# Optimization experiments

Measured on AMD Instinct MI355X. Metric: run time of the kernel, lower is better.

The kernel has to match this reference:

```python
import jax, jax.numpy as jnp
import numpy as np

N_HEADS = 16
D_EMBED = 1024
N_CROSS = 768
D_HEAD = D_EMBED // N_HEADS


def setup_inputs() -> dict:
    key = jax.random.key(0)
    ks = jax.random.split(key, 10)
    B, S = 2, 2048
    x = jax.random.normal(ks[0], (B, S, D_EMBED), dtype=jnp.float32)
    context = jax.random.normal(ks[1], (B, S, N_CROSS), dtype=jnp.float32)
    sq = 1.0 / np.sqrt(D_EMBED)
    sc = 1.0 / np.sqrt(N_CROSS)
    Wq = jax.random.normal(ks[2], (D_EMBED, D_EMBED), dtype=jnp.float32) * sq
    bq = jnp.zeros((D_EMBED,), dtype=jnp.float32)
    Wk = jax.random.normal(ks[3], (N_CROSS, D_EMBED), dtype=jnp.float32) * sc
    bk = jnp.zeros((D_EMBED,), dtype=jnp.float32)
    Wv = jax.random.normal(ks[4], (N_CROSS, D_EMBED), dtype=jnp.float32) * sc
    bv = jnp.zeros((D_EMBED,), dtype=jnp.float32)
    Wo = jax.random.normal(ks[5], (D_EMBED, D_EMBED), dtype=jnp.float32) * sq
    bo = jnp.zeros((D_EMBED,), dtype=jnp.float32)
    return {"x": x, "context": context, "Wq": Wq, "bq": bq, "Wk": Wk, "bk": bk,
            "Wv": Wv, "bv": bv, "Wo": Wo, "bo": bo}


def reference(x, context, Wq, bq, Wk, bk, Wv, bv, Wo, bo):
    B, S, _ = x.shape

    def split_heads(t):  # [B,S,E] -> [B,H,S,Dh]
        return t.reshape(B, S, N_HEADS, D_HEAD).transpose(0, 2, 1, 3)

    q = split_heads(x @ Wq + bq)
    k = split_heads(context @ Wk + bk)
    v = split_heads(context @ Wv + bv)

    scale = 1.0 / np.sqrt(D_HEAD)
    scores = jnp.einsum('bhqd,bhkd->bhqk', q, k) * scale
    attn = jax.nn.softmax(scores, axis=-1)
    out = jnp.einsum('bhqk,bhkd->bhqd', attn, v)
    out = out.transpose(0, 2, 1, 3).reshape(B, S, D_EMBED)
    return out @ Wo + bo
```

## Files before the change

### kernel.cpp

```cpp
#include <hip/hip_runtime.h>
#include <math.h>


namespace {

typedef short bfr __attribute__((ext_vector_type(8)));
typedef short s4v __attribute__((ext_vector_type(4)));
typedef unsigned u4v __attribute__((ext_vector_type(4)));
typedef float accf __attribute__((ext_vector_type(16)));

#define MFMA32(a, b, c) __builtin_amdgcn_mfma_f32_32x32x16_bf16(a, b, c, 0, 0, 0)

__device__ inline short f2bf(float f) {
    unsigned u = __float_as_uint(f);
    u += 0x7fffu + ((u >> 16) & 1u);
    return (short)(u >> 16);
}
__device__ inline float bf2f(short s) {
    return __uint_as_float(((unsigned)(unsigned short)s) << 16);
}
__device__ inline float fexp2(float x) { return __builtin_amdgcn_exp2f(x); }
__device__ inline accf zero16() {
    accf z;
#pragma unroll
    for (int i = 0; i < 16; ++i) z[i] = 0.f;
    return z;
}
__device__ inline void dma16(const void* g, void* l) {
    __builtin_amdgcn_global_load_lds(
        (const __attribute__((address_space(1))) void*)g,
        (__attribute__((address_space(3))) void*)l, 16, 0, 0);
}

__global__ __launch_bounds__(256) void prep(
    const float* __restrict__ x, const float* __restrict__ ctx,
    short* __restrict__ xb, short* __restrict__ cb,
    const float* __restrict__ Wq, const float* __restrict__ Wk,
    const float* __restrict__ Wv, const float* __restrict__ Wo,
    short* __restrict__ Wqt, short* __restrict__ Wkt,
    short* __restrict__ Wvt, short* __restrict__ Wot) {
    __shared__ short t[64][68];
    const int bx = blockIdx.x;
    if (bx < 7168) {
        int i = bx * 256 + threadIdx.x;
        if (i < 1048576) {
            float4 v = ((const float4*)x)[i];
            s4v p = {f2bf(v.x), f2bf(v.y), f2bf(v.z), f2bf(v.w)};
            ((s4v*)xb)[i] = p;
        } else {
            int j = i - 1048576;
            float4 v = ((const float4*)ctx)[j];
            s4v p = {f2bf(v.x), f2bf(v.y), f2bf(v.z), f2bf(v.w)};
            ((s4v*)cb)[j] = p;
        }
        return;
    }
    const int idx = bx - 7168;
    const int z = idx >> 8, gy = (idx >> 4) & 15, gx = idx & 15;
    const float* W;
    short* Wt;
    int K;
    switch (z) {
        case 0: W = Wq; Wt = Wqt; K = 1024; break;
        case 1: W = Wk; Wt = Wkt; K = 768; break;
        case 2: W = Wv; Wt = Wvt; K = 768; break;
        default: W = Wo; Wt = Wot; K = 1024; break;
    }
    const int k0 = gy * 64;
    if (k0 >= K) return;
    const int tid = threadIdx.x;
    const int n0 = gx * 64;
    const int kr = tid >> 4, nc = (tid & 15) * 4;
#pragma unroll
    for (int rep = 0; rep < 4; ++rep) {
        int k = kr + rep * 16;
        float4 v = *(const float4*)&W[(size_t)(k0 + k) * 1024 + n0 + nc];
        t[nc + 0][k] = f2bf(v.x);
        t[nc + 1][k] = f2bf(v.y);
        t[nc + 2][k] = f2bf(v.z);
        t[nc + 3][k] = f2bf(v.w);
    }
    __syncthreads();
    const int nr = tid >> 4, kc = (tid & 15) * 4;
#pragma unroll
    for (int rep = 0; rep < 4; ++rep) {
        int n = nr + rep * 16;
        s4v p = {t[n][kc], t[n][kc + 1], t[n][kc + 2], t[n][kc + 3]};
        *(s4v*)&Wt[(size_t)(n0 + n) * K + k0 + kc] = p;
    }
}

__global__ __launch_bounds__(256) void gemm_qkv(
    const short* __restrict__ xb, const short* __restrict__ cb,
    const short* __restrict__ Wqt, const short* __restrict__ Wkt,
    const short* __restrict__ Wvt, const float* __restrict__ bq,
    const float* __restrict__ bk, const float* __restrict__ bv,
    short* __restrict__ Qf, short* __restrict__ Kf, short* __restrict__ Vt,
    float qscale) {
    const int z = blockIdx.z;
    const short* A  = (z == 0) ? xb : cb;
    const short* Bt = (z == 0) ? Wqt : ((z == 1) ? Wkt : Wvt);
    const float* bias = (z == 0) ? bq : ((z == 1) ? bk : bv);
    const int K = (z == 0) ? 1024 : 768;
    const int NIT = K / 32;
    const float scale = (z == 0) ? qscale : 1.f;
    short* out = (z == 0) ? Qf : ((z == 1) ? Kf : Vt);

    __shared__ short As[8192];
    __shared__ short Bs[8192];
    const int t = threadIdx.x, lane = t & 63, w = t >> 6;
    const int lm = lane & 31, h2 = lane >> 5;
    const int wm = w & 1, wn = w >> 1;
    const int m0 = blockIdx.y * 128, n0 = blockIdx.x * 128;

    const int st = t ^ ((t >> 3) & 7);
    const int srow = st >> 2, scol = (st & 3) * 8;
    const short* ga = A + (size_t)(m0 + srow) * K + scol;
    const short* gb = Bt + (size_t)(n0 + srow) * K + scol;

    const int xorv = (lm >> 1) & 7;
    const int rA0 = wm * 64 + lm, rB0 = wn * 64 + lm;

    accf acc[2][2] = {zero16(), zero16(), zero16(), zero16()};

    dma16(ga, &As[w * 512]);
    dma16(ga + (size_t)64 * K, &As[2048 + w * 512]);
    dma16(gb, &Bs[w * 512]);
    dma16(gb + (size_t)64 * K, &Bs[2048 + w * 512]);

#pragma unroll 1
    for (int it = 0; it < NIT; ++it) {
        const int p = it & 1;
        __syncthreads();
        if (it + 1 < NIT) {
            const int kt = (it + 1) * 32;
            short* lA = &As[(1 - p) * 4096 + w * 512];
            short* lB = &Bs[(1 - p) * 4096 + w * 512];
            dma16(ga + kt, lA);
            dma16(ga + (size_t)64 * K + kt, lA + 2048);
            dma16(gb + kt, lB);
            dma16(gb + (size_t)64 * K + kt, lB + 2048);
        }
        const short* bA = &As[p * 4096];
        const short* bB = &Bs[p * 4096];
#pragma unroll
        for (int kk8 = 0; kk8 < 4; kk8 += 2) {
            bfr a0 = *(const bfr*)&bA[((rA0 * 4 + h2 + kk8) ^ xorv) * 8];
            bfr a1 = *(const bfr*)&bA[(((rA0 + 32) * 4 + h2 + kk8) ^ xorv) * 8];
            bfr b0 = *(const bfr*)&bB[((rB0 * 4 + h2 + kk8) ^ xorv) * 8];
            bfr b1 = *(const bfr*)&bB[(((rB0 + 32) * 4 + h2 + kk8) ^ xorv) * 8];
            acc[0][0] = MFMA32(a0, b0, acc[0][0]);
            acc[0][1] = MFMA32(a0, b1, acc[0][1]);
            acc[1][0] = MFMA32(a1, b0, acc[1][0]);
            acc[1][1] = MFMA32(a1, b1, acc[1][1]);
        }
    }

#pragma unroll
    for (int nt = 0; nt < 2; ++nt) {
        const int n = n0 + wn * 64 + nt * 32 + lm;
        const float bn = bias[n];
        const int hh = n >> 6, dd = n & 63;
#pragma unroll
        for (int mt = 0; mt < 2; ++mt) {
            const int mbase = m0 + wm * 64 + mt * 32 + 4 * h2;
            if (z != 2) {
                const int cb2 = (dd >> 4) * 512 + ((dd >> 3) & 1) * 256 + (dd & 7);
#pragma unroll
                for (int r = 0; r < 16; ++r) {
                    const int m = mbase + (r & 3) + 8 * (r >> 2);
                    const int bb = m >> 11, q = m & 2047;
                    float v = (acc[mt][nt][r] + bn) * scale;
                    out[((size_t)((bb * 16 + hh) * 64 + (q >> 5))) * 2048 +
                        cb2 + (q & 31) * 8] = f2bf(v);
                }
            } else {
                const int dblk = dd >> 5, lmv = dd & 31;
#pragma unroll
                for (int g = 0; g < 4; ++g) {
                    const int m = mbase + 8 * g;
                    const int bb = m >> 11, s = m & 2047;
                    const int kvt = s >> 6, kc = (s >> 4) & 3;
                    const int h2v = (s >> 3) & 1, j0 = s & 7;
                    s4v p = {f2bf(acc[mt][nt][4 * g + 0] + bn),
                             f2bf(acc[mt][nt][4 * g + 1] + bn),
                             f2bf(acc[mt][nt][4 * g + 2] + bn),
                             f2bf(acc[mt][nt][4 * g + 3] + bn)};
                    *(s4v*)(out +
                            ((size_t)(((bb * 16 + hh) * 32 + kvt) * 2 + dblk)) * 2048 +
                            kc * 512 + h2v * 256 + lmv * 8 + j0) = p;
                }
            }
        }
    }
}

__global__ __launch_bounds__(512) void gemm_out(
    const short* __restrict__ A, const short* __restrict__ Bt,
    const float* __restrict__ bias, float* __restrict__ out, int K) {
    __shared__ short As[8192];
    __shared__ short Bs[8192];
    const int t = threadIdx.x, lane = t & 63, w = t >> 6;
    const int lm = lane & 31, h2 = lane >> 5;
    const int wm = w & 1, wn = w >> 1;
    const int m0 = blockIdx.y * 128, n0 = blockIdx.x * 128;
    const int NIT = K / 32;

    const int st = t ^ ((t >> 3) & 7);
    const int srow = st >> 2, scol = (st & 3) * 8;
    const short* ga = A + (size_t)(m0 + srow) * K + scol;
    const short* gb = Bt + (size_t)(n0 + srow) * K + scol;

    const int xorv = (lm >> 1) & 7;
    const int rA0 = wm * 64 + lm, rB0 = wn * 32 + lm;

    accf acc[2] = {zero16(), zero16()};

    dma16(ga, &As[w * 512]);
    dma16(gb, &Bs[w * 512]);

#pragma unroll 1
    for (int it = 0; it < NIT; ++it) {
        const int p = it & 1;
        __syncthreads();
        if (it + 1 < NIT) {
            const int kt = (it + 1) * 32;
            dma16(ga + kt, &As[(1 - p) * 4096 + w * 512]);
            dma16(gb + kt, &Bs[(1 - p) * 4096 + w * 512]);
        }
        const short* bA = &As[p * 4096];
        const short* bB = &Bs[p * 4096];
#pragma unroll
        for (int kk8 = 0; kk8 < 4; kk8 += 2) {
            bfr a0 = *(const bfr*)&bA[((rA0 * 4 + h2 + kk8) ^ xorv) * 8];
            bfr a1 = *(const bfr*)&bA[(((rA0 + 32) * 4 + h2 + kk8) ^ xorv) * 8];
            bfr b0 = *(const bfr*)&bB[((rB0 * 4 + h2 + kk8) ^ xorv) * 8];
            acc[0] = MFMA32(a0, b0, acc[0]);
            acc[1] = MFMA32(a1, b0, acc[1]);
        }
    }

    const int n = n0 + wn * 32 + lm;
    const float bn = bias[n];
#pragma unroll
    for (int mt = 0; mt < 2; ++mt) {
        const int mbase = m0 + wm * 64 + mt * 32 + 4 * h2;
#pragma unroll
        for (int r = 0; r < 16; ++r) {
            const int m = mbase + (r & 3) + 8 * (r >> 2);
            out[(size_t)m * 1024 + n] = acc[mt][r] + bn;
        }
    }
}

__global__ __launch_bounds__(256, 3) void attn(
    const short* __restrict__ Qf, const short* __restrict__ Kf,
    const short* __restrict__ Vt, short* __restrict__ part,
    float* __restrict__ lsum) {
    __shared__ short smem[16384];
    const int bid = blockIdx.x;
    const int hidx = bid & 31, qs = bid >> 5;
    const int split = qs & 1, qb = qs >> 1;
    const int b = hidx >> 4, h = hidx & 15;
    const int lane = threadIdx.x & 63, wv = threadIdx.x >> 6;
    const int lm = lane & 31, h2 = lane >> 5;
    const bool hb = h2 != 0;
    const int q0 = qb * 128 + wv * 32;

    const short* qbase =
        Qf + ((size_t)(hidx * 64 + (q0 >> 5))) * 2048 + lane * 8;
    bfr qf[4];
#pragma unroll
    for (int kc = 0; kc < 4; ++kc) qf[kc] = *(const bfr*)(qbase + kc * 512);

    const short* khead = Kf + (size_t)hidx * 131072 + split * 65536;
    const short* vhead = Vt + (size_t)hidx * 131072 + split * 65536;
    const short* gsrc =
        ((wv < 2) ? (khead + wv * 2048) : (vhead + (wv - 2) * 2048)) + lane * 8;

#pragma unroll
    for (int i = 0; i < 4; ++i)
        dma16(gsrc + i * 512, &smem[wv * 2048 + i * 512]);

    accf oa0 = zero16(), oa1 = zero16();
    float la0 = 0.f, la1 = 0.f;

#pragma unroll 1
    for (int it = 0; it < 16; ++it) {
        const int p = it & 1;
        __syncthreads();
        if (it + 1 < 16) {
            const short* gn = gsrc + (size_t)(it + 1) * 4096;
            short* ln = &smem[(1 - p) * 8192 + wv * 2048];
#pragma unroll
            for (int i = 0; i < 4; ++i) dma16(gn + i * 512, ln + i * 512);
        }
        const short* kb = &smem[p * 8192];
        bfr kf0[4], kf1[4], vf0[4], vf1[4];
#pragma unroll
        for (int kc = 0; kc < 4; ++kc) {
            kf0[kc] = *(const bfr*)&kb[kc * 512 + lane * 8];
            kf1[kc] = *(const bfr*)&kb[2048 + kc * 512 + lane * 8];
            vf0[kc] = *(const bfr*)&kb[4096 + kc * 512 + lane * 8];
            vf1[kc] = *(const bfr*)&kb[6144 + kc * 512 + lane * 8];
        }
        accf s0 = zero16(), s1 = zero16();
#pragma unroll
        for (int kc = 0; kc < 4; ++kc) {
            s0 = MFMA32(kf0[kc], qf[kc], s0);
            s1 = MFMA32(kf1[kc], qf[kc], s1);
        }

#pragma unroll
        for (int i = 0; i < 16; ++i) s0[i] = fexp2(s0[i]);
#pragma unroll
        for (int i = 0; i < 16; ++i) s1[i] = fexp2(s1[i]);
#pragma unroll
        for (int i = 0; i < 16; ++i) {
            if (i & 1) la1 += s0[i] + s1[i];
            else       la0 += s0[i] + s1[i];
        }

        bfr pb[4];
#pragma unroll
        for (int kc = 0; kc < 4; ++kc) {
            const accf& s = (kc < 2) ? s0 : s1;
            const int base = 8 * (kc & 1);
            unsigned Lw0 = __builtin_amdgcn_perm(__float_as_uint(s[base + 1]),
                                                 __float_as_uint(s[base + 0]),
                                                 0x07060302u);
            unsigned Lw1 = __builtin_amdgcn_perm(__float_as_uint(s[base + 3]),
                                                 __float_as_uint(s[base + 2]),
                                                 0x07060302u);
            unsigned Hw0 = __builtin_amdgcn_perm(__float_as_uint(s[base + 5]),
                                                 __float_as_uint(s[base + 4]),
                                                 0x07060302u);
            unsigned Hw1 = __builtin_amdgcn_perm(__float_as_uint(s[base + 7]),
                                                 __float_as_uint(s[base + 6]),
                                                 0x07060302u);
            unsigned c0 = hb ? Lw0 : Hw0;
            unsigned c1 = hb ? Lw1 : Hw1;
            unsigned r0 = (unsigned)__shfl_xor((int)c0, 32);
            unsigned r1 = (unsigned)__shfl_xor((int)c1, 32);
            u4v pw = {hb ? r0 : Lw0, hb ? r1 : Lw1,
                      hb ? Hw0 : r0, hb ? Hw1 : r1};
            pb[kc] = __builtin_bit_cast(bfr, pw);
        }

#pragma unroll
        for (int kc = 0; kc < 4; ++kc) {
            oa0 = MFMA32(vf0[kc], pb[kc], oa0);
            oa1 = MFMA32(vf1[kc], pb[kc], oa1);
        }
    }

    float ls = la0 + la1;
    ls += __shfl_xor(ls, 32);
    if (!hb) lsum[((size_t)(split * 2 + b) * 16 + h) * 2048 + q0 + lm] = ls;

    short* orow = part + (size_t)split * 4194304 +
                  (size_t)(b * 2048 + q0 + lm) * 1024 + h * 64;
#pragma unroll
    for (int dt = 0; dt < 2; ++dt) {
        const accf& oa = dt ? oa1 : oa0;
#pragma unroll
        for (int g = 0; g < 4; ++g) {
            const int d0 = dt * 32 + 4 * h2 + 8 * g;
            s4v p = {f2bf(oa[4 * g + 0]), f2bf(oa[4 * g + 1]),
                     f2bf(oa[4 * g + 2]), f2bf(oa[4 * g + 3])};
            *(s4v*)(orow + d0) = p;
        }
    }
}

__global__ __launch_bounds__(256) void combine(
    const short* __restrict__ p0, const short* __restrict__ p1,
    const float* __restrict__ lsum, short* __restrict__ ao) {
    const int t = blockIdx.x * 256 + threadIdx.x;
    const int col8 = t & 127, m = t >> 7;
    const int h = col8 >> 3;
    const int b = m >> 11, q = m & 2047;
    const float l0 = lsum[((size_t)(0 + b) * 16 + h) * 2048 + q];
    const float l1 = lsum[((size_t)(2 + b) * 16 + h) * 2048 + q];
    const float inv = 1.f / (l0 + l1);
    const size_t e0 = (size_t)m * 1024 + col8 * 8;
    bfr a = *(const bfr*)(p0 + e0);
    bfr c = *(const bfr*)(p1 + e0);
    bfr r;
#pragma unroll
    for (int j = 0; j < 8; ++j) r[j] = f2bf((bf2f(a[j]) + bf2f(c[j])) * inv);
    *(bfr*)(ao + e0) = r;
}

}

extern "C" void kernel_launch(void* const* d_in, const int* in_sizes, int n_in,
                              void* d_out, int out_size, void* d_ws,
                              size_t ws_size, hipStream_t stream) {
    const float* x   = (const float*)d_in[0];
    const float* ctx = (const float*)d_in[1];
    const float* Wq  = (const float*)d_in[2];
    const float* bq  = (const float*)d_in[3];
    const float* Wk  = (const float*)d_in[4];
    const float* bk  = (const float*)d_in[5];
    const float* Wv  = (const float*)d_in[6];
    const float* bv  = (const float*)d_in[7];
    const float* Wo  = (const float*)d_in[8];
    const float* bo  = (const float*)d_in[9];

    short* xb  = (short*)d_ws;
    short* cb  = xb + (size_t)4096 * 1024;
    short* Wqt = cb + (size_t)4096 * 768;
    short* Wkt = Wqt + (size_t)1024 * 1024;
    short* Wvt = Wkt + (size_t)1024 * 768;
    short* Wot = Wvt + (size_t)1024 * 768;
    short* Qf  = Wot + (size_t)1024 * 1024;
    short* Kf  = Qf + (size_t)4096 * 1024;
    short* Vt  = Kf + (size_t)4096 * 1024;
    short* p0  = Vt + (size_t)4096 * 1024;
    short* p1  = p0 + (size_t)4096 * 1024;
    float* lsum = (float*)(p1 + (size_t)4096 * 1024);

    prep<<<8192, 256, 0, stream>>>(x, ctx, xb, cb, Wq, Wk, Wv, Wo,
                                   Wqt, Wkt, Wvt, Wot);

    const float qscale = 0.125f * 1.44269504088896f;
    gemm_qkv<<<dim3(8, 32, 3), 256, 0, stream>>>(xb, cb, Wqt, Wkt, Wvt,
                                                 bq, bk, bv, Qf, Kf, Vt,
                                                 qscale);

    attn<<<1024, 256, 0, stream>>>(Qf, Kf, Vt, p0, lsum);
    combine<<<2048, 256, 0, stream>>>(p0, p1, lsum, xb);

    gemm_out<<<dim3(8, 32), 512, 0, stream>>>(xb, Wot, bo, (float*)d_out, 1024);
}
```

Measured before the change: 216.9 us.

## Fuse split-attention combine into output GEMM A-tile load and linearize grids

Removes the separate combine kernel. The output projection GEMM now loads both attention partial buffers into registers, sums them, and scales by the per-head reciprocal of the summed softmax denominators (precomputed per row for all 16 heads). It then converts the result to bf16 and writes it into the A tile in LDS after the MFMA step, while the B tile keeps using direct DMA. Both GEMMs move to a 1D grid where the M block index changes fastest, which changes L2 reuse patterns. This saves one kernel launch and one intermediate write and read, but the A loads are now synchronous register loads with extra ALU work inside the main loop.

```diff
diff --git a/kernel.cpp b/kernel.cpp
--- a/kernel.cpp
+++ b/kernel.cpp
@@ -97,7 +97,9 @@
     const float* __restrict__ bk, const float* __restrict__ bv,
     short* __restrict__ Qf, short* __restrict__ Kf, short* __restrict__ Vt,
     float qscale) {
-    const int z = blockIdx.z;
+    const int bid = blockIdx.x;
+    const int z = bid >> 8;
+    const int local = bid & 255;
     const short* A  = (z == 0) ? xb : cb;
     const short* Bt = (z == 0) ? Wqt : ((z == 1) ? Wkt : Wvt);
     const float* bias = (z == 0) ? bq : ((z == 1) ? bk : bv);
@@ -111,7 +113,7 @@
     const int t = threadIdx.x, lane = t & 63, w = t >> 6;
     const int lm = lane & 31, h2 = lane >> 5;
     const int wm = w & 1, wn = w >> 1;
-    const int m0 = blockIdx.y * 128, n0 = blockIdx.x * 128;
+    const int m0 = (local & 31) * 128, n0 = (local >> 5) * 128;
 
     const int st = t ^ ((t >> 3) & 7);
     const int srow = st >> 2, scol = (st & 3) * 8;
@@ -196,37 +198,62 @@
 }
 
 __global__ __launch_bounds__(512) void gemm_out(
-    const short* __restrict__ A, const short* __restrict__ Bt,
-    const float* __restrict__ bias, float* __restrict__ out, int K) {
+    const short* __restrict__ p0, const short* __restrict__ p1,
+    const float* __restrict__ lsum, const short* __restrict__ Bt,
+    const float* __restrict__ bias, float* __restrict__ out) {
+    constexpr int K = 1024, NIT = 32;
     __shared__ short As[8192];
     __shared__ short Bs[8192];
     const int t = threadIdx.x, lane = t & 63, w = t >> 6;
     const int lm = lane & 31, h2 = lane >> 5;
     const int wm = w & 1, wn = w >> 1;
-    const int m0 = blockIdx.y * 128, n0 = blockIdx.x * 128;
-    const int NIT = K / 32;
+    const int bid = blockIdx.x;
+    const int m0 = (bid & 31) * 128, n0 = (bid >> 5) * 128;
 
     const int st = t ^ ((t >> 3) & 7);
     const int srow = st >> 2, scol = (st & 3) * 8;
-    const short* ga = A + (size_t)(m0 + srow) * K + scol;
+    const int gm = m0 + srow;
+    const int b = gm >> 11, q = gm & 2047;
+    const short* pa0 = p0 + (size_t)gm * 1024 + scol;
+    const short* pa1 = p1 + (size_t)gm * 1024 + scol;
     const short* gb = Bt + (size_t)(n0 + srow) * K + scol;
+
+    float inv[16];
+#pragma unroll
+    for (int h = 0; h < 16; ++h) {
+        float l0 = lsum[((size_t)b * 16 + h) * 2048 + q];
+        float l1 = lsum[((size_t)(2 + b) * 16 + h) * 2048 + q];
+        inv[h] = 1.f / (l0 + l1);
+    }
 
     const int xorv = (lm >> 1) & 7;
     const int rA0 = wm * 64 + lm, rB0 = wn * 32 + lm;
 
     accf acc[2] = {zero16(), zero16()};
 
-    dma16(ga, &As[w * 512]);
     dma16(gb, &Bs[w * 512]);
+    {
+        bfr v0 = *(const bfr*)pa0;
+        bfr v1 = *(const bfr*)pa1;
+        const float iv = inv[0];
+        bfr pk;
+#pragma unroll
+        for (int j = 0; j < 8; ++j)
+            pk[j] = f2bf((bf2f(v0[j]) + bf2f(v1[j])) * iv);
+        *(bfr*)&As[t * 8] = pk;
+    }
 
 #pragma unroll 1
     for (int it = 0; it < NIT; ++it) {
         const int p = it & 1;
         __syncthreads();
-        if (it + 1 < NIT) {
-            const int kt = (it + 1) * 32;
-            dma16(ga + kt, &As[(1 - p) * 4096 + w * 512]);
-            dma16(gb + kt, &Bs[(1 - p) * 4096 + w * 512]);
+        bfr v0, v1;
+        const bool nxt = (it + 1 < NIT);
+        if (nxt) {
+            const int ktn = (it + 1) * 32;
+            dma16(gb + ktn, &Bs[(1 - p) * 4096 + w * 512]);
+            v0 = *(const bfr*)(pa0 + ktn);
+            v1 = *(const bfr*)(pa1 + ktn);
         }
         const short* bA = &As[p * 4096];
         const short* bB = &Bs[p * 4096];
@@ -237,6 +264,14 @@
             bfr b0 = *(const bfr*)&bB[((rB0 * 4 + h2 + kk8) ^ xorv) * 8];
             acc[0] = MFMA32(a0, b0, acc[0]);
             acc[1] = MFMA32(a1, b0, acc[1]);
+        }
+        if (nxt) {
+            const float iv = inv[(it + 1) >> 1];
+            bfr pk;
+#pragma unroll
+            for (int j = 0; j < 8; ++j)
+                pk[j] = f2bf((bf2f(v0[j]) + bf2f(v1[j])) * iv);
+            *(bfr*)&As[(1 - p) * 4096 + t * 8] = pk;
         }
     }
 
@@ -373,25 +408,6 @@
     }
 }
 
-__global__ __launch_bounds__(256) void combine(
-    const short* __restrict__ p0, const short* __restrict__ p1,
-    const float* __restrict__ lsum, short* __restrict__ ao) {
-    const int t = blockIdx.x * 256 + threadIdx.x;
-    const int col8 = t & 127, m = t >> 7;
-    const int h = col8 >> 3;
-    const int b = m >> 11, q = m & 2047;
-    const float l0 = lsum[((size_t)(0 + b) * 16 + h) * 2048 + q];
-    const float l1 = lsum[((size_t)(2 + b) * 16 + h) * 2048 + q];
-    const float inv = 1.f / (l0 + l1);
-    const size_t e0 = (size_t)m * 1024 + col8 * 8;
-    bfr a = *(const bfr*)(p0 + e0);
-    bfr c = *(const bfr*)(p1 + e0);
-    bfr r;
-#pragma unroll
-    for (int j = 0; j < 8; ++j) r[j] = f2bf((bf2f(a[j]) + bf2f(c[j])) * inv);
-    *(bfr*)(ao + e0) = r;
-}
-
 }
 
 extern "C" void kernel_launch(void* const* d_in, const int* in_sizes, int n_in,
@@ -425,12 +441,10 @@
                                    Wqt, Wkt, Wvt, Wot);
 
     const float qscale = 0.125f * 1.44269504088896f;
-    gemm_qkv<<<dim3(8, 32, 3), 256, 0, stream>>>(xb, cb, Wqt, Wkt, Wvt,
-                                                 bq, bk, bv, Qf, Kf, Vt,
-                                                 qscale);
+    gemm_qkv<<<768, 256, 0, stream>>>(xb, cb, Wqt, Wkt, Wvt,
+                                      bq, bk, bv, Qf, Kf, Vt, qscale);
 
     attn<<<1024, 256, 0, stream>>>(Qf, Kf, Vt, p0, lsum);
-    combine<<<2048, 256, 0, stream>>>(p0, p1, lsum, xb);
-
-    gemm_out<<<dim3(8, 32), 512, 0, stream>>>(xb, Wot, bo, (float*)d_out, 1024);
-}
+
+    gemm_out<<<256, 512, 0, stream>>>(p0, p1, lsum, Wot, bo, (float*)d_out);
+}
```

Measured after the change: 216.7 us. No clear change (-0.1%).
